# Kernel optimization log

Measured on AMD Instinct MI355X. Metric: run time of the kernel, lower is better.

## Reference

```python
import jax, jax.numpy as jnp
import numpy as np

M, K, N = 8192, 4096, 12288


def setup_inputs() -> dict:
    key = jax.random.key(0)
    k1, k2, k3, k4 = jax.random.split(key, 4)
    input_tensor = jax.random.normal(k1, (1, M, K), dtype=jnp.float32)
    # int8 quantized weight [N, K] and per-output-channel scale [N, 1]
    weight = jax.random.randint(k2, (N, K), -127, 128, dtype=jnp.int32).astype(jnp.int8)
    weight_scale = (jax.random.uniform(k3, (N, 1), dtype=jnp.float32) * 0.01 + 1e-4)
    bias = jax.random.normal(k4, (N,), dtype=jnp.float32) * 0.1
    return {"input_tensor": input_tensor, "weight": weight,
            "weight_scale": weight_scale, "bias": bias}


def reference(input_tensor, weight, weight_scale, bias):
    x = input_tensor[0]  # squeeze(0) -> [M, K]
    # dynamic per-token symmetric int8 quantization: scale = absmax/127
    a_scale = jnp.max(jnp.abs(x), axis=-1, keepdims=True) / 127.0  # [M, 1]
    q = jnp.clip(jnp.round(x / a_scale), -128.0, 127.0)  # int8 values held in f32
    # int8 GEMM accumulated (emulated in f32), then dequant with per-token x per-channel scales
    acc = jnp.einsum('mk,nk->mn', q, weight.astype(jnp.float32))  # [M, N]
    out = acc * a_scale * weight_scale[:, 0][None, :] + bias[None, :]
    return out[None].astype(input_tensor.dtype)  # unsqueeze(0) -> [1, M, N]
```

## Files before the change

### kernel.cpp

```cpp
#include <hip/hip_runtime.h>
#include <cstdint>

#define M_DIM 8192
#define K_DIM 4096
#define N_DIM 12288
#define KT 64

using i32x4 = __attribute__((ext_vector_type(4))) int;

__device__ inline void gload_lds16(const void* g, void* l) {
    __builtin_amdgcn_global_load_lds(
        (const __attribute__((address_space(1))) void*)g,
        (__attribute__((address_space(3))) void*)l,
        16, 0, 0);
}

__global__ __launch_bounds__(256) void quant_pack(const float* __restrict__ x,
                                                  const int* __restrict__ w32,
                                                  int8_t* __restrict__ qa,
                                                  float* __restrict__ ascale,
                                                  int8_t* __restrict__ wq) {
    const int t = threadIdx.x;
    if (blockIdx.x < M_DIM) {
        const int row = blockIdx.x;
        const float4* xr = (const float4*)(x + (size_t)row * K_DIM);
        float4 v[4];
        float amax = 0.0f;
#pragma unroll
        for (int c = 0; c < 4; ++c) {
            v[c] = xr[t + 256 * c];
            amax = fmaxf(amax, fmaxf(fmaxf(fabsf(v[c].x), fabsf(v[c].y)),
                                     fmaxf(fabsf(v[c].z), fabsf(v[c].w))));
        }
#pragma unroll
        for (int off = 32; off > 0; off >>= 1)
            amax = fmaxf(amax, __shfl_xor(amax, off));
        __shared__ float smax[4];
        if ((t & 63) == 0) smax[t >> 6] = amax;
        __syncthreads();
        amax = fmaxf(fmaxf(smax[0], smax[1]), fmaxf(smax[2], smax[3]));
        const float sc = amax * (1.0f / 127.0f);
        const float inv = (amax > 0.0f) ? (127.0f / amax) : 0.0f;
        if (t == 0) ascale[row] = sc;

        int* q32 = (int*)(qa + (size_t)row * K_DIM);
#pragma unroll
        for (int c = 0; c < 4; ++c) {
            int q0 = (int)rintf(v[c].x * inv);
            int q1 = (int)rintf(v[c].y * inv);
            int q2 = (int)rintf(v[c].z * inv);
            int q3 = (int)rintf(v[c].w * inv);
            q0 = min(127, max(-128, q0));
            q1 = min(127, max(-128, q1));
            q2 = min(127, max(-128, q2));
            q3 = min(127, max(-128, q3));
            q32[t + 256 * c] = (q0 & 255) | ((q1 & 255) << 8) | ((q2 & 255) << 16) | (q3 << 24);
        }
    } else {
        const int pb = blockIdx.x - M_DIM;
        const size_t total4 = (size_t)N_DIM * K_DIM / 4;
        const size_t stride = (size_t)2048 * 256;
        int* out32 = (int*)wq;
        for (size_t i = (size_t)pb * 256 + t; i < total4; i += stride) {
            const int4 v = ((const int4*)w32)[i];
            out32[i] = (v.x & 255) | ((v.y & 255) << 8) | ((v.z & 255) << 16) | (v.w << 24);
        }
    }
}

__global__ __launch_bounds__(512, 2) void gemm_i8(const int8_t* __restrict__ qa,
                                                  const int8_t* __restrict__ wq,
                                                  const float* __restrict__ ascale,
                                                  const float* __restrict__ wscale,
                                                  const float* __restrict__ bias,
                                                  float* __restrict__ out) {
    __shared__ int8_t lds[4][2][16384];

    const int t = threadIdx.x;
    const int lane = t & 63;
    const int wave = t >> 6;
    const int wm = wave >> 2;
    const int wn = wave & 3;
    const int lrow = lane & 15;
    const int lk = lane >> 4;
    const int rslot = (lk ^ ((lrow >> 1) & 3)) << 4;

    const int flat = blockIdx.x;
    const int sw = (flat & 7) * 192 + (flat >> 3);
    const int bm = sw / 48;
    const int bn = sw % 48;

    const int g = (t & 3) ^ ((t >> 3) & 3);
    const size_t aoff0 = (size_t)(bm * 256 + (t >> 2)) * K_DIM + (size_t)g * 16;
    const size_t aoff1 = aoff0 + (size_t)128 * K_DIM;
    const size_t boff0 = (size_t)(bn * 256 + (t >> 2)) * K_DIM + (size_t)g * 16;
    const size_t boff1 = boff0 + (size_t)128 * K_DIM;

#define STAGE_A(sb, jt)                                                        \
    {                                                                          \
        gload_lds16(qa + aoff0 + (size_t)(jt) * 64, &lds[sb][0][t * 16]);      \
        gload_lds16(qa + aoff1 + (size_t)(jt) * 64, &lds[sb][0][t * 16 + 8192]); \
    }
#define STAGE_B(sb, jt)                                                        \
    {                                                                          \
        gload_lds16(wq + boff0 + (size_t)(jt) * 64, &lds[sb][1][t * 16]);      \
        gload_lds16(wq + boff1 + (size_t)(jt) * 64, &lds[sb][1][t * 16 + 8192]); \
    }

#define READ_AHI(s)                                                            \
    {                                                                          \
        _Pragma("unroll") for (int mf = 0; mf < 4; ++mf)                       \
            ahi[mf] = *(const i32x4*)&lds[s][0][(wm * 128 + (mf + 4) * 16 +    \
                                                lrow) * 64 + rslot];           \
    }
#define READ_NEXT(s, ALO, BN)                                                  \
    {                                                                          \
        _Pragma("unroll") for (int nf = 0; nf < 4; ++nf)                       \
            BN[nf] = *(const i32x4*)&lds[s][1][(wn * 64 + nf * 16 + lrow) * 64 + rslot]; \
        _Pragma("unroll") for (int mf = 0; mf < 4; ++mf)                       \
            ALO[mf] = *(const i32x4*)&lds[s][0][(wm * 128 + mf * 16 + lrow) * 64 + rslot]; \
    }
#define MMLO(ALO, BC)                                                          \
    {                                                                          \
        __builtin_amdgcn_s_setprio(1);                                         \
        _Pragma("unroll") for (int mf = 0; mf < 4; ++mf)                       \
            _Pragma("unroll") for (int nf = 0; nf < 4; ++nf)                   \
                acc[mf][nf] = __builtin_amdgcn_mfma_i32_16x16x64_i8(           \
                    ALO[mf], BC[nf], acc[mf][nf], 0, 0, 0);                    \
        __builtin_amdgcn_s_setprio(0);                                         \
    }
#define MMHI(BC)                                                               \
    {                                                                          \
        __builtin_amdgcn_s_setprio(1);                                         \
        _Pragma("unroll") for (int mf = 0; mf < 4; ++mf)                       \
            _Pragma("unroll") for (int nf = 0; nf < 4; ++nf)                   \
                acc[mf + 4][nf] = __builtin_amdgcn_mfma_i32_16x16x64_i8(       \
                    ahi[mf], BC[nf], acc[mf + 4][nf], 0, 0, 0);                \
        __builtin_amdgcn_s_setprio(0);                                         \
    }
#define SB0 __builtin_amdgcn_sched_barrier(0);
#define BAR __builtin_amdgcn_s_barrier();
#define WAIT_LGKM(n) asm volatile("s_waitcnt lgkmcnt(" #n ")" ::: "memory");
#define WAIT_VM(n) asm volatile("s_waitcnt vmcnt(" #n ")" ::: "memory");

#define PH0(J, ALO, BC)                                                        \
    {                                                                          \
        READ_AHI((J) & 3);                                                     \
        STAGE_A(((J) + 2) & 3, (J) + 2);                                       \
        WAIT_VM(2);                                                            \
        SB0;                                                                   \
        BAR;                                                                   \
        WAIT_LGKM(4);                                                          \
        SB0;                                                                   \
        MMLO(ALO, BC);                                                         \
    }
#define PH1(J, BC, ALON, BN)                                                   \
    {                                                                          \
        READ_NEXT(((J) + 1) & 3, ALON, BN);                                    \
        STAGE_B(((J) + 2) & 3, (J) + 2);                                       \
        SB0;                                                                   \
        BAR;                                                                   \
        WAIT_LGKM(8);                                                          \
        SB0;                                                                   \
        MMHI(BC);                                                              \
    }

    i32x4 acc[8][4] = {};
    i32x4 alo0[4], b0[4], alo1[4], b1[4], ahi[4];

    STAGE_A(0, 0);
    STAGE_B(0, 0);
    STAGE_A(1, 1);
    STAGE_B(1, 1);
    WAIT_VM(4);
    SB0;
    BAR;
    READ_NEXT(0, alo0, b0);

    for (int jp = 0; jp < 31; ++jp) {
        const int j = jp * 2;
        PH0(j, alo0, b0);
        PH1(j, b0, alo1, b1);
        PH0(j + 1, alo1, b1);
        PH1(j + 1, b1, alo0, b0);
    }

    {
        READ_AHI(62 & 3);
        WAIT_VM(0);
        SB0;
        BAR;
        WAIT_LGKM(4);
        SB0;
        MMLO(alo0, b0);

        READ_NEXT(63 & 3, alo1, b1);
        SB0;
        BAR;
        WAIT_LGKM(8);
        SB0;
        MMHI(b0);
    }
    {
        READ_AHI(63 & 3);
        WAIT_LGKM(4);
        SB0;
        MMLO(alo1, b1);
        WAIT_LGKM(0);
        SB0;
        MMHI(b1);
    }

    const int r0 = bm * 256 + wm * 128;
    const int c0 = bn * 256 + wn * 64;
    float asc[8][4];
#pragma unroll
    for (int m = 0; m < 8; ++m)
#pragma unroll
        for (int jj = 0; jj < 4; ++jj)
            asc[m][jj] = ascale[r0 + m * 16 + lk * 4 + jj];
#pragma unroll
    for (int n = 0; n < 4; ++n) {
        const int col = c0 + n * 16 + lrow;
        const float wsc = wscale[col];
        const float bb = bias[col];
#pragma unroll
        for (int m = 0; m < 8; ++m) {
#pragma unroll
            for (int jj = 0; jj < 4; ++jj) {
                const int row = r0 + m * 16 + lk * 4 + jj;
                out[(size_t)row * N_DIM + col] = (float)acc[m][n][jj] * asc[m][jj] * wsc + bb;
            }
        }
    }
}

extern "C" void kernel_launch(void* const* d_in, const int* in_sizes, int n_in,
                              void* d_out, int out_size, void* d_ws, size_t ws_size,
                              hipStream_t stream) {
    const float* x = (const float*)d_in[0];
    const int* w32 = (const int*)d_in[1];
    const float* wscale = (const float*)d_in[2];
    const float* bias = (const float*)d_in[3];
    float* out = (float*)d_out;

    int8_t* qa = (int8_t*)d_ws;
    float* ascale = (float*)((char*)d_ws + (size_t)M_DIM * K_DIM);
    int8_t* wq = (int8_t*)((char*)d_ws + (size_t)M_DIM * K_DIM +
                           (size_t)M_DIM * sizeof(float));

    quant_pack<<<M_DIM + 2048, 256, 0, stream>>>(x, w32, qa, ascale, wq);
    gemm_i8<<<1536, 512, 0, stream>>>(qa, wq, ascale, wscale, bias, out);
}
```

Baseline: 537.7 us.

## Restructure GEMM main loop into 3-deep prefetch with interleaved LDS reads

```diff
diff --git a/kernel.cpp b/kernel.cpp
--- a/kernel.cpp
+++ b/kernel.cpp
@@ -96,119 +96,90 @@
     const size_t boff0 = (size_t)(bn * 256 + (t >> 2)) * K_DIM + (size_t)g * 16;
     const size_t boff1 = boff0 + (size_t)128 * K_DIM;
 
-#define STAGE_A(sb, jt)                                                        \
+#define STAGE_ALL(sb, jt)                                                      \
     {                                                                          \
         gload_lds16(qa + aoff0 + (size_t)(jt) * 64, &lds[sb][0][t * 16]);      \
         gload_lds16(qa + aoff1 + (size_t)(jt) * 64, &lds[sb][0][t * 16 + 8192]); \
-    }
-#define STAGE_B(sb, jt)                                                        \
-    {                                                                          \
         gload_lds16(wq + boff0 + (size_t)(jt) * 64, &lds[sb][1][t * 16]);      \
         gload_lds16(wq + boff1 + (size_t)(jt) * 64, &lds[sb][1][t * 16 + 8192]); \
     }
 
-#define READ_AHI(s)                                                            \
-    {                                                                          \
-        _Pragma("unroll") for (int mf = 0; mf < 4; ++mf)                       \
-            ahi[mf] = *(const i32x4*)&lds[s][0][(wm * 128 + (mf + 4) * 16 +    \
-                                                lrow) * 64 + rslot];           \
-    }
-#define READ_NEXT(s, ALO, BN)                                                  \
-    {                                                                          \
+#define READS(S, NA, NB)                                                       \
+    _Pragma("unroll") for (int nf = 0; nf < 4; ++nf)                           \
+        NB[nf] = *(const i32x4*)&lds[S][1][(wn * 64 + nf * 16 + lrow) * 64 + rslot]; \
+    _Pragma("unroll") for (int mf = 0; mf < 8; ++mf)                           \
+        NA[mf] = *(const i32x4*)&lds[S][0][(wm * 128 + mf * 16 + lrow) * 64 + rslot];
+
+#define MFMA32(CA, CB)                                                         \
+    _Pragma("unroll") for (int mf = 0; mf < 8; ++mf)                           \
         _Pragma("unroll") for (int nf = 0; nf < 4; ++nf)                       \
-            BN[nf] = *(const i32x4*)&lds[s][1][(wn * 64 + nf * 16 + lrow) * 64 + rslot]; \
-        _Pragma("unroll") for (int mf = 0; mf < 4; ++mf)                       \
-            ALO[mf] = *(const i32x4*)&lds[s][0][(wm * 128 + mf * 16 + lrow) * 64 + rslot]; \
-    }
-#define MMLO(ALO, BC)                                                          \
-    {                                                                          \
-        __builtin_amdgcn_s_setprio(1);                                         \
-        _Pragma("unroll") for (int mf = 0; mf < 4; ++mf)                       \
-            _Pragma("unroll") for (int nf = 0; nf < 4; ++nf)                   \
-                acc[mf][nf] = __builtin_amdgcn_mfma_i32_16x16x64_i8(           \
-                    ALO[mf], BC[nf], acc[mf][nf], 0, 0, 0);                    \
-        __builtin_amdgcn_s_setprio(0);                                         \
-    }
-#define MMHI(BC)                                                               \
-    {                                                                          \
-        __builtin_amdgcn_s_setprio(1);                                         \
-        _Pragma("unroll") for (int mf = 0; mf < 4; ++mf)                       \
-            _Pragma("unroll") for (int nf = 0; nf < 4; ++nf)                   \
-                acc[mf + 4][nf] = __builtin_amdgcn_mfma_i32_16x16x64_i8(       \
-                    ahi[mf], BC[nf], acc[mf + 4][nf], 0, 0, 0);                \
-        __builtin_amdgcn_s_setprio(0);                                         \
-    }
+            acc[mf][nf] = __builtin_amdgcn_mfma_i32_16x16x64_i8(               \
+                CA[mf], CB[nf], acc[mf][nf], 0, 0, 0);
+
+#define SGBPAT                                                                 \
+    _Pragma("unroll") for (int c = 0; c < 4; ++c) {                            \
+        __builtin_amdgcn_sched_group_barrier(0x008, 8, 0);                     \
+        __builtin_amdgcn_sched_group_barrier(0x100, 3, 0);                     \
+    }
+
 #define SB0 __builtin_amdgcn_sched_barrier(0);
 #define BAR __builtin_amdgcn_s_barrier();
 #define WAIT_LGKM(n) asm volatile("s_waitcnt lgkmcnt(" #n ")" ::: "memory");
 #define WAIT_VM(n) asm volatile("s_waitcnt vmcnt(" #n ")" ::: "memory");
 
-#define PH0(J, ALO, BC)                                                        \
+#define TILE_MAIN(J, CA, CB, NA, NB)                                           \
     {                                                                          \
-        READ_AHI((J) & 3);                                                     \
-        STAGE_A(((J) + 2) & 3, (J) + 2);                                       \
-        WAIT_VM(2);                                                            \
+        STAGE_ALL(((J) + 3) & 3, (J) + 3);                                     \
+        WAIT_VM(8);                                                            \
+        BAR;                                                                   \
+        __builtin_amdgcn_s_setprio(1);                                         \
+        READS(((J) + 1) & 3, NA, NB);                                          \
+        MFMA32(CA, CB);                                                        \
+        SGBPAT;                                                                \
+        __builtin_amdgcn_s_setprio(0);                                         \
+        WAIT_LGKM(0);                                                          \
         SB0;                                                                   \
+    }
+#define TILE_TAIL(VMN, S, CA, CB, NA, NB)                                      \
+    {                                                                          \
+        WAIT_VM(VMN);                                                          \
         BAR;                                                                   \
-        WAIT_LGKM(4);                                                          \
+        __builtin_amdgcn_s_setprio(1);                                         \
+        READS(S, NA, NB);                                                      \
+        MFMA32(CA, CB);                                                        \
+        SGBPAT;                                                                \
+        __builtin_amdgcn_s_setprio(0);                                         \
+        WAIT_LGKM(0);                                                          \
         SB0;                                                                   \
-        MMLO(ALO, BC);                                                         \
-    }
-#define PH1(J, BC, ALON, BN)                                                   \
-    {                                                                          \
-        READ_NEXT(((J) + 1) & 3, ALON, BN);                                    \
-        STAGE_B(((J) + 2) & 3, (J) + 2);                                       \
-        SB0;                                                                   \
-        BAR;                                                                   \
-        WAIT_LGKM(8);                                                          \
-        SB0;                                                                   \
-        MMHI(BC);                                                              \
     }
 
     i32x4 acc[8][4] = {};
-    i32x4 alo0[4], b0[4], alo1[4], b1[4], ahi[4];
-
-    STAGE_A(0, 0);
-    STAGE_B(0, 0);
-    STAGE_A(1, 1);
-    STAGE_B(1, 1);
-    WAIT_VM(4);
+    i32x4 fa0[8], fb0[4], fa1[8], fb1[4];
+
+    STAGE_ALL(0, 0);
+    STAGE_ALL(1, 1);
+    STAGE_ALL(2, 2);
+    WAIT_VM(8);
+    BAR;
+    READS(0, fa0, fb0);
+    WAIT_LGKM(0);
     SB0;
-    BAR;
-    READ_NEXT(0, alo0, b0);
-
-    for (int jp = 0; jp < 31; ++jp) {
+
+    for (int jp = 0; jp < 30; ++jp) {
         const int j = jp * 2;
-        PH0(j, alo0, b0);
-        PH1(j, b0, alo1, b1);
-        PH0(j + 1, alo1, b1);
-        PH1(j + 1, b1, alo0, b0);
-    }
-
+        TILE_MAIN(j, fa0, fb0, fa1, fb1);
+        TILE_MAIN(j + 1, fa1, fb1, fa0, fb0);
+    }
     {
-        READ_AHI(62 & 3);
-        WAIT_VM(0);
-        SB0;
-        BAR;
-        WAIT_LGKM(4);
-        SB0;
-        MMLO(alo0, b0);
-
-        READ_NEXT(63 & 3, alo1, b1);
-        SB0;
-        BAR;
-        WAIT_LGKM(8);
-        SB0;
-        MMHI(b0);
-    }
+        STAGE_ALL(3, 63);
+        TILE_TAIL(8, 61 & 3, fa0, fb0, fa1, fb1);
+    }
+    TILE_TAIL(4, 62 & 3, fa1, fb1, fa0, fb0);
+    TILE_TAIL(0, 63 & 3, fa0, fb0, fa1, fb1);
     {
-        READ_AHI(63 & 3);
-        WAIT_LGKM(4);
-        SB0;
-        MMLO(alo1, b1);
-        WAIT_LGKM(0);
-        SB0;
-        MMHI(b1);
+        __builtin_amdgcn_s_setprio(1);
+        MFMA32(fa1, fb1);
+        __builtin_amdgcn_s_setprio(0);
     }
 
     const int r0 = bm * 256 + wm * 128;
```

Result: no change. 541.7 us (+0.7%).
